# Performance work log

Measured on AMD Instinct MI355X. Metric: run time of the kernel, lower is better.

The kernel has to match this reference:

```python
import jax, jax.numpy as jnp
import numpy as np

BC = 256   # block_channel
NB0, NB1 = 4, 2  # blocks per modality (1024/256, 512/256)
EPS = 1e-5

def setup_inputs() -> dict:
    key = jax.random.key(0)
    ks = jax.random.split(key, 8)
    B, C0, C1, L = 16, 1024, 512, 2048
    RC = 64
    x0 = jax.random.normal(ks[0], (B, C0, L), jnp.float32)
    x1 = jax.random.normal(ks[1], (B, C1, L), jnp.float32)
    W_joint = jax.random.normal(ks[2], (RC, BC), jnp.float32) * 0.05
    b_joint = jax.random.normal(ks[3], (RC,), jnp.float32) * 0.05
    bn_gamma = jnp.ones((RC,), jnp.float32)
    bn_beta = jnp.zeros((RC,), jnp.float32)
    bn_mean = jnp.zeros((RC,), jnp.float32)
    bn_var = jnp.ones((RC,), jnp.float32)
    W_group = jax.random.normal(ks[4], (NB0 + NB1, BC, RC), jnp.float32) * 0.05
    b_group = jax.random.normal(ks[5], (NB0 + NB1, BC), jnp.float32) * 0.05
    return {"x0": x0, "x1": x1, "W_joint": W_joint, "b_joint": b_joint,
            "bn_gamma": bn_gamma, "bn_beta": bn_beta, "bn_mean": bn_mean,
            "bn_var": bn_var, "W_group": W_group, "b_group": b_group}

def reference(x0, x1, W_joint, b_joint, bn_gamma, bn_beta, bn_mean, bn_var, W_group, b_group):
    B, C0, L = x0.shape
    _, C1, _ = x1.shape
    # split channels into blocks of BC (divisible -> pad branch is a no-op)
    xb0 = x0.reshape(B, NB0, BC, L)
    xb1 = x1.reshape(B, NB1, BC, L)
    # per-modality block-sum, GAP over spatial, then sum over modalities -> [B, BC]
    gap = (xb0.sum(axis=1) + xb1.sum(axis=1)).mean(axis=-1)
    # joint features: Linear -> BatchNorm1d (eval, running stats) -> ReLU
    h = gap @ W_joint.T + b_joint
    h = (h - bn_mean) * jax.lax.rsqrt(bn_var + EPS) * bn_gamma + bn_beta
    h = jax.nn.relu(h)  # [B, RC]
    # grouped per-block linears as one batched GEMM, softmax over blocks (axis 0)
    logits = jnp.einsum('br,kcr->kbc', h, W_group) + b_group[:, None, :]  # [K, B, BC]
    atten = jax.nn.softmax(logits, axis=0)  # lowest_atten = 0 -> att = atten
    a0 = jnp.transpose(atten[:NB0], (1, 0, 2))[..., None]  # [B, NB0, BC, 1]
    a1 = jnp.transpose(atten[NB0:], (1, 0, 2))[..., None]
    out0 = (xb0 * a0).reshape(B, C0, L)
    out1 = (xb1 * a1).reshape(B, C1, L)
    return (out0, out1)
```

## Files before the change

kernel.cpp:

```cpp
#include <hip/hip_runtime.h>

#define BB   16
#define C0   1024
#define C1   512
#define LEN  2048
#define BC   256
#define RC   64
#define NB0  4
#define NB1  2
#define KK   6
#define EPSV 1e-5f

__global__ __launch_bounds__(256) void gap_kernel(const float* __restrict__ x0,
                                                  const float* __restrict__ x1,
                                                  float* __restrict__ gap) {
    const int c = blockIdx.x;
    const int b = blockIdx.y;
    const int t = threadIdx.x;

    const float4* rows[KK];
#pragma unroll
    for (int k = 0; k < NB0; ++k)
        rows[k] = (const float4*)(x0 + ((size_t)b * C0 + (size_t)k * BC + c) * LEN);
#pragma unroll
    for (int k = 0; k < NB1; ++k)
        rows[NB0 + k] = (const float4*)(x1 + ((size_t)b * C1 + (size_t)k * BC + c) * LEN);

    float s = 0.f;
#pragma unroll
    for (int k = 0; k < KK; ++k) {
        float4 v0 = rows[k][t];
        float4 v1 = rows[k][t + 256];
        s += (v0.x + v0.y) + (v0.z + v0.w) + (v1.x + v1.y) + (v1.z + v1.w);
    }
#pragma unroll
    for (int off = 32; off > 0; off >>= 1)
        s += __shfl_down(s, off, 64);
    __shared__ float ws_[4];
    if ((t & 63) == 0) ws_[t >> 6] = s;
    __syncthreads();
    if (t == 0) {
        float tot = (ws_[0] + ws_[1]) + (ws_[2] + ws_[3]);
        gap[b * BC + c] = tot * (1.0f / (float)LEN);
    }
}

__global__ __launch_bounds__(256) void atten_kernel(const float* __restrict__ gap,
                                                    const float* __restrict__ Wj,
                                                    const float* __restrict__ bj,
                                                    const float* __restrict__ gamma,
                                                    const float* __restrict__ beta,
                                                    const float* __restrict__ mean,
                                                    const float* __restrict__ var,
                                                    const float* __restrict__ Wg,
                                                    const float* __restrict__ bg,
                                                    float* __restrict__ atten) {
    const int b = blockIdx.x;
    const int t = threadIdx.x;
    __shared__ float g_s[BC];
    __shared__ float h_s[RC];

    g_s[t] = gap[b * BC + t];
    __syncthreads();

    if (t < RC) {
        float acc = 0.f;
        const float* w = Wj + (size_t)t * BC;
        for (int c = 0; c < BC; ++c) acc = fmaf(g_s[c], w[c], acc);
        acc += bj[t];
        acc = (acc - mean[t]) * rsqrtf(var[t] + EPSV) * gamma[t] + beta[t];
        h_s[t] = fmaxf(acc, 0.f);
    }
    __syncthreads();

    float logit[KK];
#pragma unroll
    for (int k = 0; k < KK; ++k) {
        float acc = bg[k * BC + t];
        const float* w = Wg + ((size_t)k * BC + t) * RC;
#pragma unroll 8
        for (int r = 0; r < RC; ++r) acc = fmaf(h_s[r], w[r], acc);
        logit[k] = acc;
    }
    float m = logit[0];
#pragma unroll
    for (int k = 1; k < KK; ++k) m = fmaxf(m, logit[k]);
    float sum = 0.f;
#pragma unroll
    for (int k = 0; k < KK; ++k) { logit[k] = expf(logit[k] - m); sum += logit[k]; }
    const float inv = 1.f / sum;
#pragma unroll
    for (int k = 0; k < KK; ++k)
        atten[((size_t)k * BB + b) * BC + t] = logit[k] * inv;
}

__global__ __launch_bounds__(256) void scale_kernel(const float* __restrict__ x0,
                                                    const float* __restrict__ x1,
                                                    const float* __restrict__ atten,
                                                    float* __restrict__ out) {
    const int row = blockIdx.x;
    const int b  = row / (C0 + C1);
    const int ch = row - b * (C0 + C1);
    const int t  = threadIdx.x;

    const float4* src;
    float4* dst;
    float scale;
    if (ch < C0) {
        const int k = ch >> 8, c = ch & 255;
        scale = atten[((size_t)k * BB + b) * BC + c];
        src = (const float4*)(x0 + ((size_t)b * C0 + ch) * LEN);
        dst = (float4*)(out + ((size_t)b * C0 + ch) * LEN);
    } else {
        const int ch1 = ch - C0;
        const int k = NB0 + (ch1 >> 8), c = ch1 & 255;
        scale = atten[((size_t)k * BB + b) * BC + c];
        src = (const float4*)(x1 + ((size_t)b * C1 + ch1) * LEN);
        dst = (float4*)(out + (size_t)BB * C0 * LEN + ((size_t)b * C1 + ch1) * LEN);
    }
    float4 v0 = src[t];
    float4 v1 = src[t + 256];
    v0.x *= scale; v0.y *= scale; v0.z *= scale; v0.w *= scale;
    v1.x *= scale; v1.y *= scale; v1.z *= scale; v1.w *= scale;
    dst[t] = v0;
    dst[t + 256] = v1;
}

extern "C" void kernel_launch(void* const* d_in, const int* in_sizes, int n_in,
                              void* d_out, int out_size, void* d_ws, size_t ws_size,
                              hipStream_t stream) {
    const float* x0    = (const float*)d_in[0];
    const float* x1    = (const float*)d_in[1];
    const float* Wj    = (const float*)d_in[2];
    const float* bj    = (const float*)d_in[3];
    const float* gamma = (const float*)d_in[4];
    const float* beta  = (const float*)d_in[5];
    const float* mean  = (const float*)d_in[6];
    const float* var   = (const float*)d_in[7];
    const float* Wg    = (const float*)d_in[8];
    const float* bg    = (const float*)d_in[9];
    float* out = (float*)d_out;

    float* ws    = (float*)d_ws;
    float* gap   = ws;
    float* atten = ws + 4096;

    gap_kernel<<<dim3(BC, BB), 256, 0, stream>>>(x0, x1, gap);
    atten_kernel<<<BB, 256, 0, stream>>>(gap, Wj, bj, gamma, beta, mean, var, Wg, bg, atten);
    scale_kernel<<<BB * (C0 + C1), 256, 0, stream>>>(x0, x1, atten, out);
}
```

Measured before the change: 402.7 us.

## Use nontemporal output stores, wave-parallel joint linear, and native vector types

The scale kernel now writes its output with nontemporal stores through ext_vector_type float4, so the large output stream is meant to avoid polluting the cache. The joint linear in the attention kernel is spread across all four waves, with a shuffle reduction per output row instead of 64 serial threads. The group GEMV loop is fully unrolled and the softmax uses the fast __expf. The main kernels are memory-bound, so the gain probably rests on the nontemporal stores, while the attention tweaks only touch a tiny kernel.

```diff
diff --git a/kernel.cpp b/kernel.cpp
--- a/kernel.cpp
+++ b/kernel.cpp
@@ -11,6 +11,8 @@
 #define KK   6
 #define EPSV 1e-5f
 
+typedef float vfloat4 __attribute__((ext_vector_type(4)));
+
 __global__ __launch_bounds__(256) void gap_kernel(const float* __restrict__ x0,
                                                   const float* __restrict__ x1,
                                                   float* __restrict__ gap) {
@@ -18,19 +20,19 @@
     const int b = blockIdx.y;
     const int t = threadIdx.x;
 
-    const float4* rows[KK];
+    const vfloat4* rows[KK];
 #pragma unroll
     for (int k = 0; k < NB0; ++k)
-        rows[k] = (const float4*)(x0 + ((size_t)b * C0 + (size_t)k * BC + c) * LEN);
+        rows[k] = (const vfloat4*)(x0 + ((size_t)b * C0 + (size_t)k * BC + c) * LEN);
 #pragma unroll
     for (int k = 0; k < NB1; ++k)
-        rows[NB0 + k] = (const float4*)(x1 + ((size_t)b * C1 + (size_t)k * BC + c) * LEN);
+        rows[NB0 + k] = (const vfloat4*)(x1 + ((size_t)b * C1 + (size_t)k * BC + c) * LEN);
 
     float s = 0.f;
 #pragma unroll
     for (int k = 0; k < KK; ++k) {
-        float4 v0 = rows[k][t];
-        float4 v1 = rows[k][t + 256];
+        vfloat4 v0 = rows[k][t];
+        vfloat4 v1 = rows[k][t + 256];
         s += (v0.x + v0.y) + (v0.z + v0.w) + (v1.x + v1.y) + (v1.z + v1.w);
     }
 #pragma unroll
@@ -55,21 +57,32 @@
                                                     const float* __restrict__ Wg,
                                                     const float* __restrict__ bg,
                                                     float* __restrict__ atten) {
-    const int b = blockIdx.x;
-    const int t = threadIdx.x;
+    const int b    = blockIdx.x;
+    const int t    = threadIdx.x;
+    const int lane = t & 63;
+    const int wave = t >> 6;
     __shared__ float g_s[BC];
     __shared__ float h_s[RC];
 
     g_s[t] = gap[b * BC + t];
     __syncthreads();
 
-    if (t < RC) {
-        float acc = 0.f;
-        const float* w = Wj + (size_t)t * BC;
-        for (int c = 0; c < BC; ++c) acc = fmaf(g_s[c], w[c], acc);
-        acc += bj[t];
-        acc = (acc - mean[t]) * rsqrtf(var[t] + EPSV) * gamma[t] + beta[t];
-        h_s[t] = fmaxf(acc, 0.f);
+#pragma unroll
+    for (int i = 0; i < 16; ++i) {
+        const int r = wave * 16 + i;
+        const float* w = Wj + (size_t)r * BC;
+        float acc = fmaf(w[lane], g_s[lane],
+                    fmaf(w[lane + 64], g_s[lane + 64],
+                    fmaf(w[lane + 128], g_s[lane + 128],
+                         w[lane + 192] * g_s[lane + 192])));
+#pragma unroll
+        for (int off = 32; off > 0; off >>= 1)
+            acc += __shfl_down(acc, off, 64);
+        if (lane == 0) {
+            float v = acc + bj[r];
+            v = (v - mean[r]) * rsqrtf(var[r] + EPSV) * gamma[r] + beta[r];
+            h_s[r] = fmaxf(v, 0.f);
+        }
     }
     __syncthreads();
 
@@ -78,7 +91,7 @@
     for (int k = 0; k < KK; ++k) {
         float acc = bg[k * BC + t];
         const float* w = Wg + ((size_t)k * BC + t) * RC;
-#pragma unroll 8
+#pragma unroll
         for (int r = 0; r < RC; ++r) acc = fmaf(h_s[r], w[r], acc);
         logit[k] = acc;
     }
@@ -87,7 +100,7 @@
     for (int k = 1; k < KK; ++k) m = fmaxf(m, logit[k]);
     float sum = 0.f;
 #pragma unroll
-    for (int k = 0; k < KK; ++k) { logit[k] = expf(logit[k] - m); sum += logit[k]; }
+    for (int k = 0; k < KK; ++k) { logit[k] = __expf(logit[k] - m); sum += logit[k]; }
     const float inv = 1.f / sum;
 #pragma unroll
     for (int k = 0; k < KK; ++k)
@@ -103,27 +116,27 @@
     const int ch = row - b * (C0 + C1);
     const int t  = threadIdx.x;
 
-    const float4* src;
-    float4* dst;
+    const vfloat4* src;
+    vfloat4* dst;
     float scale;
     if (ch < C0) {
         const int k = ch >> 8, c = ch & 255;
         scale = atten[((size_t)k * BB + b) * BC + c];
-        src = (const float4*)(x0 + ((size_t)b * C0 + ch) * LEN);
-        dst = (float4*)(out + ((size_t)b * C0 + ch) * LEN);
+        src = (const vfloat4*)(x0 + ((size_t)b * C0 + ch) * LEN);
+        dst = (vfloat4*)(out + ((size_t)b * C0 + ch) * LEN);
     } else {
         const int ch1 = ch - C0;
         const int k = NB0 + (ch1 >> 8), c = ch1 & 255;
         scale = atten[((size_t)k * BB + b) * BC + c];
-        src = (const float4*)(x1 + ((size_t)b * C1 + ch1) * LEN);
-        dst = (float4*)(out + (size_t)BB * C0 * LEN + ((size_t)b * C1 + ch1) * LEN);
+        src = (const vfloat4*)(x1 + ((size_t)b * C1 + ch1) * LEN);
+        dst = (vfloat4*)(out + (size_t)BB * C0 * LEN + ((size_t)b * C1 + ch1) * LEN);
     }
-    float4 v0 = src[t];
-    float4 v1 = src[t + 256];
-    v0.x *= scale; v0.y *= scale; v0.z *= scale; v0.w *= scale;
-    v1.x *= scale; v1.y *= scale; v1.z *= scale; v1.w *= scale;
-    dst[t] = v0;
-    dst[t + 256] = v1;
+    vfloat4 v0 = src[t];
+    vfloat4 v1 = src[t + 256];
+    v0 *= scale;
+    v1 *= scale;
+    __builtin_nontemporal_store(v0, &dst[t]);
+    __builtin_nontemporal_store(v1, &dst[t + 256]);
 }
 
 extern "C" void kernel_launch(void* const* d_in, const int* in_sizes, int n_in,
```

Result: no change. 400.2 us (-0.6%).
